# Kernel tuning notes

Hardware: AMD Instinct MI355X
Metric: run time of the kernel (lower is better)

Reference implementation:

```python
import jax, jax.numpy as jnp
import numpy as np

C = 1.0            # curvature
MIN_NORM = 1e-15   # hgcn min_norm
PROJ_EPS = 4e-3    # hgcn PoincareBall float32 boundary eps
N, D, E = 100000, 128, 1600000


def _artanh(x):
    # hgcn Artanh clamps input away from +-1 for stability
    return jnp.arctanh(jnp.clip(x, -1.0 + 1e-5, 1.0 - 1e-5))


def logmap0(p, c):
    sqrt_c = c ** 0.5
    p_norm = jnp.maximum(jnp.linalg.norm(p, axis=-1, keepdims=True), MIN_NORM)
    return p * _artanh(sqrt_c * p_norm) / (sqrt_c * p_norm)


def expmap0(u, c):
    sqrt_c = c ** 0.5
    u_norm = jnp.maximum(jnp.linalg.norm(u, axis=-1, keepdims=True), MIN_NORM)
    return jnp.tanh(sqrt_c * u_norm) * u / (sqrt_c * u_norm)


def proj(x, c):
    norm = jnp.maximum(jnp.linalg.norm(x, axis=-1, keepdims=True), MIN_NORM)
    maxnorm = (1.0 - PROJ_EPS) / (c ** 0.5)
    return jnp.where(norm > maxnorm, x / norm * maxnorm, x)


def setup_inputs() -> dict:
    key = jax.random.key(0)
    k1, k2, k3, k4 = jax.random.split(key, 4)
    # node features on the Poincare ball (small tangent vectors -> exp -> proj)
    x = proj(0.05 * jax.random.normal(k1, (N, D), dtype=jnp.float32), C)
    rows = jax.random.randint(k2, (E,), 0, N, dtype=jnp.int32)   # dst nodes
    cols = jax.random.randint(k3, (E,), 0, N, dtype=jnp.int32)   # src nodes
    # positive edge weights, roughly row-normalized (avg degree 16)
    vals = jax.random.uniform(k4, (E,), dtype=jnp.float32) / 16.0
    return {"x": x, "rows": rows, "cols": cols, "vals": vals}


def reference(x, rows, cols, vals):
    # x_tangent = logmap0(x)
    x_tangent = logmap0(x, C)                         # [N, D]
    # support_t = spmm(adj, x_tangent): gather src features, weight, scatter-add to dst
    msgs = vals[:, None] * x_tangent[cols]            # [E, D]
    support_t = jax.ops.segment_sum(msgs, rows, num_segments=N)  # [N, D]
    # output = proj(expmap0(support_t))
    return proj(expmap0(support_t, C), C)
```

## Files before the change

kernel.cpp:

```cpp
#include <hip/hip_runtime.h>
#include <hip/hip_fp16.h>
#include <math.h>

#define DIM 128
#define MAXNORM (1.0f - 4e-3f)
#define RPB 128
#define EPB 4096
#define CAP 64
#define CSTRIDE 32
#define SCAN_BLK 1024
#define GTHREADS 512

__device__ __forceinline__ float wave_reduce_sum(float v) {
    #pragma unroll
    for (int off = 32; off > 0; off >>= 1)
        v += __shfl_xor(v, off, 64);
    return v;
}

__device__ __forceinline__ float bf_lo(unsigned u) { return __uint_as_float(u << 16); }
__device__ __forceinline__ float bf_hi(unsigned u) { return __uint_as_float(u & 0xffff0000u); }

__device__ __forceinline__ unsigned pack_bf2(float a, float b) {
    unsigned ua = __float_as_uint(a), ub = __float_as_uint(b);
    ua += 0x7fffu + ((ua >> 16) & 1u);
    ub += 0x7fffu + ((ub >> 16) & 1u);
    return (ua >> 16) | (ub & 0xffff0000u);
}

__global__ void xt_kernel(const float* __restrict__ x,
                          unsigned* __restrict__ xt, int n) {
    int wave = (int)((blockIdx.x * blockDim.x + threadIdx.x) >> 6);
    int lane = threadIdx.x & 63;
    if (wave >= n) return;
    const float2* xr = (const float2*)(x + (size_t)wave * DIM);
    float2 v = xr[lane];
    float ss = wave_reduce_sum(v.x * v.x + v.y * v.y);
    float norm = sqrtf(ss);
    float t = fminf(norm, 1.0f - 1e-5f);
    float at = 0.5f * logf((1.0f + t) / (1.0f - t));
    float f = at / fmaxf(norm, 1e-15f);
    xt[(size_t)wave * 64 + lane] = pack_bf2(v.x * f, v.y * f);
}

__global__ void hist_part_kernel(const int* __restrict__ rows,
                                 int* __restrict__ hist, int E, int NB) {
    extern __shared__ int lh[];
    int tid = threadIdx.x;
    for (int i = tid; i < NB; i += 256) lh[i] = 0;
    __syncthreads();
    int base = blockIdx.x * EPB;
    for (int k = 0; k < EPB; k += 256) {
        int e = base + k + tid;
        if (e < E) atomicAdd(&lh[rows[e] >> 7], 1);
    }
    __syncthreads();
    int* h = hist + (size_t)blockIdx.x * NB;
    for (int i = tid; i < NB; i += 256) h[i] = lh[i];
}

__global__ void colscan_kernel(int* __restrict__ hist, int* __restrict__ bucketTotal,
                               int NEB, int NB) {
    int b = blockIdx.x * 64 + threadIdx.x;
    if (b >= NB) return;
    int carry = 0;
    int blk = 0;
    for (; blk + 8 <= NEB; blk += 8) {
        int v[8];
        #pragma unroll
        for (int k = 0; k < 8; k++) v[k] = hist[(size_t)(blk + k) * NB + b];
        #pragma unroll
        for (int k = 0; k < 8; k++) { hist[(size_t)(blk + k) * NB + b] = carry; carry += v[k]; }
    }
    for (; blk < NEB; blk++) {
        int v = hist[(size_t)blk * NB + b];
        hist[(size_t)blk * NB + b] = carry; carry += v;
    }
    bucketTotal[b] = carry;
}

__global__ void excl_scan_kernel(const int* __restrict__ src, int* __restrict__ dst, int nb) {
    __shared__ int s[SCAN_BLK];
    int tid = threadIdx.x;
    int v0 = (tid < nb) ? src[tid] : 0;
    s[tid] = v0; __syncthreads();
    for (int off = 1; off < SCAN_BLK; off <<= 1) {
        int v = (tid >= off) ? s[tid - off] : 0; __syncthreads();
        s[tid] += v; __syncthreads();
    }
    if (tid < nb) dst[tid] = s[tid] - v0;
}

__global__ void reorder_kernel(const int* __restrict__ rows, const int* __restrict__ cols,
                               const float* __restrict__ vals,
                               const int* __restrict__ hist,
                               const int* __restrict__ bucketBase,
                               uint2* __restrict__ records, int E, int NB) {
    extern __shared__ int sm[];
    int* s        = sm;
    int* locStart = sm + SCAN_BLK;
    int* locCur   = locStart + NB;
    int* gbase    = locCur + NB;
    uint2* stage  = (uint2*)(gbase + NB);
    int tid = threadIdx.x;
    int base = blockIdx.x * EPB;
    int nloc = E - base; if (nloc > EPB) nloc = EPB;

    for (int i = tid; i < NB; i += SCAN_BLK) locCur[i] = 0;
    __syncthreads();
    for (int k = 0; k < EPB; k += SCAN_BLK) {
        int e = base + k + tid;
        if (e < E) atomicAdd(&locCur[rows[e] >> 7], 1);
    }
    __syncthreads();
    int v0 = (tid < NB) ? locCur[tid] : 0;
    s[tid] = v0; __syncthreads();
    for (int off = 1; off < SCAN_BLK; off <<= 1) {
        int v = (tid >= off) ? s[tid - off] : 0; __syncthreads();
        s[tid] += v; __syncthreads();
    }
    int excl = s[tid] - v0;
    if (tid < NB) {
        locStart[tid] = excl;
        locCur[tid]   = excl;
        gbase[tid]    = bucketBase[tid] + hist[(size_t)blockIdx.x * NB + tid];
    }
    __syncthreads();
    for (int k = 0; k < EPB; k += SCAN_BLK) {
        int e = base + k + tid;
        if (e < E) {
            int r = rows[e];
            int b = r >> 7;
            unsigned hw = (unsigned)__half_as_ushort(__float2half(vals[e])) & 0x7fffu;
            unsigned pk = ((unsigned)cols[e] << 15) | hw;
            int p = atomicAdd(&locCur[b], 1);
            stage[p] = make_uint2(pk, (unsigned)r);
        }
    }
    __syncthreads();
    for (int i = tid; i < nloc; i += SCAN_BLK) {
        uint2 rec = stage[i];
        int b = (int)(rec.y >> 7);
        int rank = i - locStart[b];
        records[(size_t)gbase[b] + rank] = rec;
    }
}

__global__ void bucket_gather_kernel(const unsigned* __restrict__ xt,
                                     const uint2* __restrict__ records,
                                     const int* __restrict__ bucketBase,
                                     const int* __restrict__ bucketTotal,
                                     float* __restrict__ out, int n) {
    __shared__ unsigned ell[RPB * CAP];
    __shared__ int cnt[RPB];
    int b = blockIdx.x;
    int tid = threadIdx.x;
    int row0 = b * RPB;
    int rowsInB = n - row0; if (rowsInB > RPB) rowsInB = RPB;
    for (int i = tid; i < RPB; i += GTHREADS) cnt[i] = 0;
    __syncthreads();
    int e0 = bucketBase[b];
    int e1 = e0 + bucketTotal[b];
    for (int i = e0 + tid; i < e1; i += GTHREADS) {
        uint2 rec = records[i];
        int lr = (int)(rec.y & (RPB - 1));
        int p = atomicAdd(&cnt[lr], 1);
        if (p < CAP) ell[lr * CAP + p] = rec.x;
    }
    __syncthreads();
    int wv = tid >> 6, lane = tid & 63;
    for (int lr = wv; lr < rowsInB; lr += GTHREADS / 64) {
        int deg = cnt[lr]; if (deg > CAP) deg = CAP;
        float2 acc = make_float2(0.f, 0.f);
        const unsigned* erow = &ell[lr * CAP];
        for (int j = 0; j < deg; j += 8) {
            float w[8]; unsigned u[8]; int c[8];
            #pragma unroll
            for (int k = 0; k < 8; k++) {
                int idx = j + k;
                bool ok = idx < deg;
                unsigned p = erow[ok ? idx : 0];
                c[k] = (int)(p >> 15);
                w[k] = ok ? __half2float(__ushort_as_half((unsigned short)(p & 0x7fffu))) : 0.f;
            }
            #pragma unroll
            for (int k = 0; k < 8; k++) u[k] = xt[(size_t)c[k] * 64 + lane];
            #pragma unroll
            for (int k = 0; k < 8; k++) {
                acc.x = fmaf(w[k], bf_lo(u[k]), acc.x);
                acc.y = fmaf(w[k], bf_hi(u[k]), acc.y);
            }
        }
        float ss = wave_reduce_sum(acc.x * acc.x + acc.y * acc.y);
        float n0 = fmaxf(sqrtf(ss), 1e-15f);
        float th = tanhf(n0);
        float f = (th > MAXNORM) ? (MAXNORM / n0) : (th / n0);
        float2* o = (float2*)(out + (size_t)(row0 + lr) * DIM);
        o[lane] = make_float2(acc.x * f, acc.y * f);
    }
}

__global__ void scatter_ell_kernel(const int* __restrict__ rows,
                                   const int* __restrict__ cols,
                                   const float* __restrict__ vals,
                                   int* __restrict__ cur,
                                   unsigned* __restrict__ ell, int E) {
    int e = blockIdx.x * blockDim.x + threadIdx.x;
    if (e >= E) return;
    int r = rows[e];
    unsigned hb = (unsigned)__half_as_ushort(__float2half(vals[e])) & 0x7fffu;
    unsigned pk = ((unsigned)cols[e] << 15) | hb;
    int pos = atomicAdd(&cur[(size_t)r * CSTRIDE], 1);
    if (pos < CAP) ell[(size_t)r * CAP + pos] = pk;
}

__global__ void gather_ell_kernel(const unsigned* __restrict__ xt,
                                  const unsigned* __restrict__ ell,
                                  const int* __restrict__ cur,
                                  float* __restrict__ out, int n) {
    int wave = (int)((blockIdx.x * blockDim.x + threadIdx.x) >> 6);
    int lane = threadIdx.x & 63;
    if (wave >= n) return;
    int deg = cur[(size_t)wave * CSTRIDE];
    if (deg > CAP) deg = CAP;
    unsigned pl = 0;
    if (lane < deg) pl = ell[(size_t)wave * CAP + lane];
    float2 acc = make_float2(0.f, 0.f);
    for (int j = 0; j < deg; j += 8) {
        float w[8]; unsigned u[8]; int c[8];
        #pragma unroll
        for (int k = 0; k < 8; k++) {
            int idx = j + k;
            bool ok = idx < deg;
            unsigned p = __shfl(pl, ok ? idx : 0);
            c[k] = (int)(p >> 15);
            w[k] = ok ? __half2float(__ushort_as_half((unsigned short)(p & 0x7fffu))) : 0.f;
        }
        #pragma unroll
        for (int k = 0; k < 8; k++)
            u[k] = xt[(size_t)c[k] * 64 + lane];
        #pragma unroll
        for (int k = 0; k < 8; k++) {
            acc.x = fmaf(w[k], bf_lo(u[k]), acc.x);
            acc.y = fmaf(w[k], bf_hi(u[k]), acc.y);
        }
    }
    float ss = wave_reduce_sum(acc.x * acc.x + acc.y * acc.y);
    float n0 = fmaxf(sqrtf(ss), 1e-15f);
    float th = tanhf(n0);
    float f = (th > MAXNORM) ? (MAXNORM / n0) : (th / n0);
    float2* o = (float2*)(out + (size_t)wave * DIM);
    o[lane] = make_float2(acc.x * f, acc.y * f);
}

__global__ void tangent_kernel(const float* __restrict__ x,
                               float* __restrict__ xt, int n) {
    int wave = (int)((blockIdx.x * blockDim.x + threadIdx.x) >> 6);
    int lane = threadIdx.x & 63;
    if (wave >= n) return;
    const float2* xr = (const float2*)(x + (size_t)wave * DIM);
    float2 v = xr[lane];
    float ss = wave_reduce_sum(v.x * v.x + v.y * v.y);
    float norm = sqrtf(ss);
    float t = fminf(norm, 1.0f - 1e-5f);
    float at = 0.5f * logf((1.0f + t) / (1.0f - t));
    float factor = at / fmaxf(norm, 1e-15f);
    float2* o = (float2*)(xt + (size_t)wave * DIM);
    o[lane] = make_float2(v.x * factor, v.y * factor);
}

__global__ void scatter_kernel(const float* __restrict__ xt,
                               const int* __restrict__ rows,
                               const int* __restrict__ cols,
                               const float* __restrict__ vals,
                               float* __restrict__ out, int E) {
    long gid = (long)blockIdx.x * blockDim.x + threadIdx.x;
    int e = (int)(gid >> 5);
    int lane = (int)(gid & 31);
    if (e >= E) return;
    int r = rows[e];
    int c = cols[e];
    float w = vals[e];
    const float4* src = (const float4*)(xt + (size_t)c * DIM);
    float4 v = src[lane];
    float* dst = out + (size_t)r * DIM + lane * 4;
    unsafeAtomicAdd(dst + 0, v.x * w);
    unsafeAtomicAdd(dst + 1, v.y * w);
    unsafeAtomicAdd(dst + 2, v.z * w);
    unsafeAtomicAdd(dst + 3, v.w * w);
}

__global__ void finalize_kernel(float* __restrict__ out, int n) {
    int wave = (int)((blockIdx.x * blockDim.x + threadIdx.x) >> 6);
    int lane = threadIdx.x & 63;
    if (wave >= n) return;
    float2* p = (float2*)(out + (size_t)wave * DIM);
    float2 v = p[lane];
    float ss = wave_reduce_sum(v.x * v.x + v.y * v.y);
    float n0 = fmaxf(sqrtf(ss), 1e-15f);
    float th = tanhf(n0);
    float factor = (th > MAXNORM) ? (MAXNORM / n0) : (th / n0);
    p[lane] = make_float2(v.x * factor, v.y * factor);
}

extern "C" void kernel_launch(void* const* d_in, const int* in_sizes, int n_in,
                              void* d_out, int out_size, void* d_ws, size_t ws_size,
                              hipStream_t stream) {
    const float* x    = (const float*)d_in[0];
    const int*   rows = (const int*)d_in[1];
    const int*   cols = (const int*)d_in[2];
    const float* vals = (const float*)d_in[3];
    float* out = (float*)d_out;

    int n = in_sizes[0] / DIM;
    int E = in_sizes[1];
    int NB  = (n + RPB - 1) / RPB;
    int NEB = (E + EPB - 1) / EPB;

    auto align256 = [](size_t b) { return (b + 255) & ~(size_t)255; };

    size_t xt_b   = align256((size_t)n * 64 * 4);
    size_t rec_b  = align256((size_t)E * 8);
    size_t hist_b = align256((size_t)NEB * NB * 4);
    size_t bt_b   = align256((size_t)NB * 4);
    size_t bb_b   = align256((size_t)NB * 4);
    size_t radix_need = xt_b + rec_b + hist_b + bt_b + bb_b;
    size_t reorder_lds = (size_t)(SCAN_BLK + 3 * NB) * 4 + (size_t)EPB * 8;

    if (n <= (1 << 17) && NB <= SCAN_BLK && E > 0 &&
        reorder_lds <= 64 * 1024 && radix_need <= ws_size) {
        unsigned* xt_bf = (unsigned*)d_ws;
        uint2*    recs  = (uint2*)((char*)d_ws + xt_b);
        int*      hist  = (int*)((char*)d_ws + xt_b + rec_b);
        int*      btot  = (int*)((char*)d_ws + xt_b + rec_b + hist_b);
        int*      bbase = (int*)((char*)d_ws + xt_b + rec_b + hist_b + bt_b);

        xt_kernel<<<(n + 3) / 4, 256, 0, stream>>>(x, xt_bf, n);
        hist_part_kernel<<<NEB, 256, NB * 4, stream>>>(rows, hist, E, NB);
        colscan_kernel<<<(NB + 63) / 64, 64, 0, stream>>>(hist, btot, NEB, NB);
        excl_scan_kernel<<<1, SCAN_BLK, 0, stream>>>(btot, bbase, NB);
        reorder_kernel<<<NEB, SCAN_BLK, reorder_lds, stream>>>(rows, cols, vals,
                                                               hist, bbase, recs, E, NB);
        bucket_gather_kernel<<<NB, GTHREADS, 0, stream>>>(xt_bf, recs, bbase, btot, out, n);
        return;
    }

    size_t ell_b = align256((size_t)n * CAP * 4);
    size_t cur_b = align256((size_t)n * CSTRIDE * 4);
    if (n <= (1 << 17) && xt_b + ell_b + cur_b <= ws_size) {
        unsigned* xt_bf = (unsigned*)d_ws;
        unsigned* ell   = (unsigned*)((char*)d_ws + xt_b);
        int*      cur   = (int*)((char*)d_ws + xt_b + ell_b);
        xt_kernel<<<(n + 3) / 4, 256, 0, stream>>>(x, xt_bf, n);
        hipMemsetAsync(cur, 0, (size_t)n * CSTRIDE * 4, stream);
        scatter_ell_kernel<<<(E + 255) / 256, 256, 0, stream>>>(rows, cols, vals, cur, ell, E);
        gather_ell_kernel<<<(n + 3) / 4, 256, 0, stream>>>(xt_bf, ell, cur, out, n);
        return;
    }

    float* xtf = (float*)d_in[0];
    size_t xtb = (size_t)n * DIM * sizeof(float);
    if (ws_size >= xtb) xtf = (float*)d_ws;
    tangent_kernel<<<(n + 3) / 4, 256, 0, stream>>>(x, xtf, n);
    hipMemsetAsync(d_out, 0, (size_t)n * DIM * sizeof(float), stream);
    long threads = (long)E * 32;
    scatter_kernel<<<(int)((threads + 255) / 256), 256, 0, stream>>>(xtf, rows, cols, vals, out, E);
    finalize_kernel<<<(n + 3) / 4, 256, 0, stream>>>(out, n);
}
```

Measured before the change: 239.6 us.

## Use fp16 tangent features, atomic bucket offsets, and split gather blocks

Tangent features are now stored as fp16 pairs instead of bf16. The per-block histogram with its column scan is replaced by global atomic bucket totals and atomic cursor reservation in the reorder pass, which drops two kernels and the hist buffer. The gather kernel now runs two blocks per bucket, each handling 64 rows. It uses launch bounds, zero-pads ELL rows so they can be read with vectorized uint4 loads, and computes byte offsets directly. In exchange, each record list is read twice, edge order within a bucket is no longer deterministic, and fp16 has a narrower range than bf16.

```diff
diff --git a/kernel.cpp b/kernel.cpp
--- a/kernel.cpp
+++ b/kernel.cpp
@@ -5,6 +5,7 @@
 #define DIM 128
 #define MAXNORM (1.0f - 4e-3f)
 #define RPB 128
+#define GRPB 64
 #define EPB 4096
 #define CAP 64
 #define CSTRIDE 32
@@ -18,14 +19,10 @@
     return v;
 }
 
-__device__ __forceinline__ float bf_lo(unsigned u) { return __uint_as_float(u << 16); }
-__device__ __forceinline__ float bf_hi(unsigned u) { return __uint_as_float(u & 0xffff0000u); }
-
-__device__ __forceinline__ unsigned pack_bf2(float a, float b) {
-    unsigned ua = __float_as_uint(a), ub = __float_as_uint(b);
-    ua += 0x7fffu + ((ua >> 16) & 1u);
-    ub += 0x7fffu + ((ub >> 16) & 1u);
-    return (ua >> 16) | (ub & 0xffff0000u);
+__device__ __forceinline__ unsigned pack_h2(float a, float b) {
+    unsigned lo = (unsigned)__half_as_ushort(__float2half_rn(a));
+    unsigned hi = (unsigned)__half_as_ushort(__float2half_rn(b));
+    return lo | (hi << 16);
 }
 
 __global__ void xt_kernel(const float* __restrict__ x,
@@ -40,11 +37,11 @@
     float t = fminf(norm, 1.0f - 1e-5f);
     float at = 0.5f * logf((1.0f + t) / (1.0f - t));
     float f = at / fmaxf(norm, 1e-15f);
-    xt[(size_t)wave * 64 + lane] = pack_bf2(v.x * f, v.y * f);
-}
-
-__global__ void hist_part_kernel(const int* __restrict__ rows,
-                                 int* __restrict__ hist, int E, int NB) {
+    xt[(size_t)wave * 64 + lane] = pack_h2(v.x * f, v.y * f);
+}
+
+__global__ void hist_atomic_kernel(const int* __restrict__ rows,
+                                   int* __restrict__ btot, int E, int NB) {
     extern __shared__ int lh[];
     int tid = threadIdx.x;
     for (int i = tid; i < NB; i += 256) lh[i] = 0;
@@ -55,46 +52,27 @@
         if (e < E) atomicAdd(&lh[rows[e] >> 7], 1);
     }
     __syncthreads();
-    int* h = hist + (size_t)blockIdx.x * NB;
-    for (int i = tid; i < NB; i += 256) h[i] = lh[i];
-}
-
-__global__ void colscan_kernel(int* __restrict__ hist, int* __restrict__ bucketTotal,
-                               int NEB, int NB) {
-    int b = blockIdx.x * 64 + threadIdx.x;
-    if (b >= NB) return;
-    int carry = 0;
-    int blk = 0;
-    for (; blk + 8 <= NEB; blk += 8) {
-        int v[8];
-        #pragma unroll
-        for (int k = 0; k < 8; k++) v[k] = hist[(size_t)(blk + k) * NB + b];
-        #pragma unroll
-        for (int k = 0; k < 8; k++) { hist[(size_t)(blk + k) * NB + b] = carry; carry += v[k]; }
-    }
-    for (; blk < NEB; blk++) {
-        int v = hist[(size_t)blk * NB + b];
-        hist[(size_t)blk * NB + b] = carry; carry += v;
-    }
-    bucketTotal[b] = carry;
-}
-
-__global__ void excl_scan_kernel(const int* __restrict__ src, int* __restrict__ dst, int nb) {
+    for (int i = tid; i < NB; i += 256)
+        if (lh[i]) atomicAdd(&btot[i], lh[i]);
+}
+
+__global__ void scan_init_kernel(const int* __restrict__ btot,
+                                 int* __restrict__ bbase,
+                                 int* __restrict__ bcur, int nb) {
     __shared__ int s[SCAN_BLK];
     int tid = threadIdx.x;
-    int v0 = (tid < nb) ? src[tid] : 0;
+    int v0 = (tid < nb) ? btot[tid] : 0;
     s[tid] = v0; __syncthreads();
     for (int off = 1; off < SCAN_BLK; off <<= 1) {
         int v = (tid >= off) ? s[tid - off] : 0; __syncthreads();
         s[tid] += v; __syncthreads();
     }
-    if (tid < nb) dst[tid] = s[tid] - v0;
+    if (tid < nb) { int e = s[tid] - v0; bbase[tid] = e; bcur[tid] = e; }
 }
 
 __global__ void reorder_kernel(const int* __restrict__ rows, const int* __restrict__ cols,
                                const float* __restrict__ vals,
-                               const int* __restrict__ hist,
-                               const int* __restrict__ bucketBase,
+                               int* __restrict__ bucketCur,
                                uint2* __restrict__ records, int E, int NB) {
     extern __shared__ int sm[];
     int* s        = sm;
@@ -123,7 +101,7 @@
     if (tid < NB) {
         locStart[tid] = excl;
         locCur[tid]   = excl;
-        gbase[tid]    = bucketBase[tid] + hist[(size_t)blockIdx.x * NB + tid];
+        gbase[tid]    = atomicAdd(&bucketCur[tid], v0);
     }
     __syncthreads();
     for (int k = 0; k < EPB; k += SCAN_BLK) {
@@ -146,57 +124,70 @@
     }
 }
 
-__global__ void bucket_gather_kernel(const unsigned* __restrict__ xt,
-                                     const uint2* __restrict__ records,
-                                     const int* __restrict__ bucketBase,
-                                     const int* __restrict__ bucketTotal,
-                                     float* __restrict__ out, int n) {
-    __shared__ unsigned ell[RPB * CAP];
-    __shared__ int cnt[RPB];
-    int b = blockIdx.x;
+__global__ void __launch_bounds__(GTHREADS, 8)
+bucket_gather_kernel(const unsigned* __restrict__ xt,
+                     const uint2* __restrict__ records,
+                     const int* __restrict__ bucketBase,
+                     const int* __restrict__ bucketTotal,
+                     float* __restrict__ out, int n) {
+    __shared__ unsigned ell[GRPB * CAP];
+    __shared__ int cnt[GRPB];
+    int g = blockIdx.x;
+    int b = g >> 1, h = g & 1;
     int tid = threadIdx.x;
-    int row0 = b * RPB;
-    int rowsInB = n - row0; if (rowsInB > RPB) rowsInB = RPB;
-    for (int i = tid; i < RPB; i += GTHREADS) cnt[i] = 0;
+    int row0 = b * RPB + h * GRPB;
+    int rowsInB = n - row0; if (rowsInB > GRPB) rowsInB = GRPB;
+    for (int i = tid; i < GRPB; i += GTHREADS) cnt[i] = 0;
     __syncthreads();
     int e0 = bucketBase[b];
     int e1 = e0 + bucketTotal[b];
     for (int i = e0 + tid; i < e1; i += GTHREADS) {
         uint2 rec = records[i];
-        int lr = (int)(rec.y & (RPB - 1));
-        int p = atomicAdd(&cnt[lr], 1);
-        if (p < CAP) ell[lr * CAP + p] = rec.x;
+        if ((int)((rec.y >> 6) & 1u) == h) {
+            int lr = (int)(rec.y & (GRPB - 1));
+            int p = atomicAdd(&cnt[lr], 1);
+            if (p < CAP) ell[lr * CAP + p] = rec.x;
+        }
+    }
+    __syncthreads();
+    if (tid < GRPB) {
+        int d = cnt[tid]; if (d > CAP) d = CAP;
+        int dp = (d + 7) & ~7; if (dp > CAP) dp = CAP;
+        for (int ss = d; ss < dp; ++ss) ell[tid * CAP + ss] = 0;
     }
     __syncthreads();
     int wv = tid >> 6, lane = tid & 63;
+    unsigned lane4 = (unsigned)(lane << 2);
     for (int lr = wv; lr < rowsInB; lr += GTHREADS / 64) {
         int deg = cnt[lr]; if (deg > CAP) deg = CAP;
-        float2 acc = make_float2(0.f, 0.f);
+        float ax = 0.f, ay = 0.f;
         const unsigned* erow = &ell[lr * CAP];
         for (int j = 0; j < deg; j += 8) {
-            float w[8]; unsigned u[8]; int c[8];
+            uint4 qa = *(const uint4*)(erow + j);
+            uint4 qb = *(const uint4*)(erow + j + 4);
+            unsigned pk[8] = {qa.x, qa.y, qa.z, qa.w, qb.x, qb.y, qb.z, qb.w};
+            __half2 u[8];
+            float w[8];
             #pragma unroll
             for (int k = 0; k < 8; k++) {
-                int idx = j + k;
-                bool ok = idx < deg;
-                unsigned p = erow[ok ? idx : 0];
-                c[k] = (int)(p >> 15);
-                w[k] = ok ? __half2float(__ushort_as_half((unsigned short)(p & 0x7fffu))) : 0.f;
+                unsigned voff = ((pk[k] >> 15) << 8) + lane4;
+                u[k] = *(const __half2*)((const char*)xt + voff);
             }
             #pragma unroll
-            for (int k = 0; k < 8; k++) u[k] = xt[(size_t)c[k] * 64 + lane];
+            for (int k = 0; k < 8; k++)
+                w[k] = __half2float(__ushort_as_half((unsigned short)(pk[k] & 0x7fffu)));
             #pragma unroll
             for (int k = 0; k < 8; k++) {
-                acc.x = fmaf(w[k], bf_lo(u[k]), acc.x);
-                acc.y = fmaf(w[k], bf_hi(u[k]), acc.y);
+                ax = fmaf(w[k], __low2float(u[k]), ax);
+                ay = fmaf(w[k], __high2float(u[k]), ay);
             }
         }
-        float ss = wave_reduce_sum(acc.x * acc.x + acc.y * acc.y);
-        float n0 = fmaxf(sqrtf(ss), 1e-15f);
+        float ssum = wave_reduce_sum(ax * ax + ay * ay);
+        float n0 = fmaxf(sqrtf(ssum), 1e-15f);
         float th = tanhf(n0);
         float f = (th > MAXNORM) ? (MAXNORM / n0) : (th / n0);
         float2* o = (float2*)(out + (size_t)(row0 + lr) * DIM);
-        o[lane] = make_float2(acc.x * f, acc.y * f);
+        o[lane] = make_float2(ax * f, ay * f);
     }
 }
 
@@ -221,13 +212,14 @@
     int wave = (int)((blockIdx.x * blockDim.x + threadIdx.x) >> 6);
     int lane = threadIdx.x & 63;
     if (wave >= n) return;
+    const __half2* xt2 = (const __half2*)xt;
     int deg = cur[(size_t)wave * CSTRIDE];
     if (deg > CAP) deg = CAP;
     unsigned pl = 0;
     if (lane < deg) pl = ell[(size_t)wave * CAP + lane];
     float2 acc = make_float2(0.f, 0.f);
     for (int j = 0; j < deg; j += 8) {
-        float w[8]; unsigned u[8]; int c[8];
+        float w[8]; __half2 u[8]; int c[8];
         #pragma unroll
         for (int k = 0; k < 8; k++) {
             int idx = j + k;
@@ -238,11 +230,11 @@
         }
         #pragma unroll
         for (int k = 0; k < 8; k++)
-            u[k] = xt[(size_t)c[k] * 64 + lane];
+            u[k] = xt2[(size_t)c[k] * 64 + lane];
         #pragma unroll
         for (int k = 0; k < 8; k++) {
-            acc.x = fmaf(w[k], bf_lo(u[k]), acc.x);
-            acc.y = fmaf(w[k], bf_hi(u[k]), acc.y);
+            acc.x = fmaf(w[k], __low2float(u[k]), acc.x);
+            acc.y = fmaf(w[k], __high2float(u[k]), acc.y);
         }
     }
     float ss = wave_reduce_sum(acc.x * acc.x + acc.y * acc.y);
@@ -319,42 +311,40 @@
 
     auto align256 = [](size_t b) { return (b + 255) & ~(size_t)255; };
 
-    size_t xt_b   = align256((size_t)n * 64 * 4);
-    size_t rec_b  = align256((size_t)E * 8);
-    size_t hist_b = align256((size_t)NEB * NB * 4);
-    size_t bt_b   = align256((size_t)NB * 4);
-    size_t bb_b   = align256((size_t)NB * 4);
-    size_t radix_need = xt_b + rec_b + hist_b + bt_b + bb_b;
+    size_t xt_b  = align256((size_t)n * 64 * 4);
+    size_t rec_b = align256((size_t)E * 8);
+    size_t nb_b  = align256((size_t)NB * 4);
+    size_t radix_need = xt_b + rec_b + 3 * nb_b;
     size_t reorder_lds = (size_t)(SCAN_BLK + 3 * NB) * 4 + (size_t)EPB * 8;
 
     if (n <= (1 << 17) && NB <= SCAN_BLK && E > 0 &&
         reorder_lds <= 64 * 1024 && radix_need <= ws_size) {
-        unsigned* xt_bf = (unsigned*)d_ws;
+        unsigned* xt_h  = (unsigned*)d_ws;
         uint2*    recs  = (uint2*)((char*)d_ws + xt_b);
-        int*      hist  = (int*)((char*)d_ws + xt_b + rec_b);
-        int*      btot  = (int*)((char*)d_ws + xt_b + rec_b + hist_b);
-        int*      bbase = (int*)((char*)d_ws + xt_b + rec_b + hist_b + bt_b);
-
-        xt_kernel<<<(n + 3) / 4, 256, 0, stream>>>(x, xt_bf, n);
-        hist_part_kernel<<<NEB, 256, NB * 4, stream>>>(rows, hist, E, NB);
-        colscan_kernel<<<(NB + 63) / 64, 64, 0, stream>>>(hist, btot, NEB, NB);
-        excl_scan_kernel<<<1, SCAN_BLK, 0, stream>>>(btot, bbase, NB);
+        int*      btot  = (int*)((char*)d_ws + xt_b + rec_b);
+        int*      bbase = (int*)((char*)d_ws + xt_b + rec_b + nb_b);
+        int*      bcur  = (int*)((char*)d_ws + xt_b + rec_b + 2 * nb_b);
+
+        hipMemsetAsync(btot, 0, (size_t)NB * 4, stream);
+        xt_kernel<<<(n + 3) / 4, 256, 0, stream>>>(x, xt_h, n);
+        hist_atomic_kernel<<<NEB, 256, NB * 4, stream>>>(rows, btot, E, NB);
+        scan_init_kernel<<<1, SCAN_BLK, 0, stream>>>(btot, bbase, bcur, NB);
         reorder_kernel<<<NEB, SCAN_BLK, reorder_lds, stream>>>(rows, cols, vals,
-                                                               hist, bbase, recs, E, NB);
-        bucket_gather_kernel<<<NB, GTHREADS, 0, stream>>>(xt_bf, recs, bbase, btot, out, n);
+                                                               bcur, recs, E, NB);
+        bucket_gather_kernel<<<NB * 2, GTHREADS, 0, stream>>>(xt_h, recs, bbase, btot, out, n);
         return;
     }
 
     size_t ell_b = align256((size_t)n * CAP * 4);
     size_t cur_b = align256((size_t)n * CSTRIDE * 4);
     if (n <= (1 << 17) && xt_b + ell_b + cur_b <= ws_size) {
-        unsigned* xt_bf = (unsigned*)d_ws;
-        unsigned* ell   = (unsigned*)((char*)d_ws + xt_b);
-        int*      cur   = (int*)((char*)d_ws + xt_b + ell_b);
-        xt_kernel<<<(n + 3) / 4, 256, 0, stream>>>(x, xt_bf, n);
+        unsigned* xt_h = (unsigned*)d_ws;
+        unsigned* ell  = (unsigned*)((char*)d_ws + xt_b);
+        int*      cur  = (int*)((char*)d_ws + xt_b + ell_b);
+        xt_kernel<<<(n + 3) / 4, 256, 0, stream>>>(x, xt_h, n);
         hipMemsetAsync(cur, 0, (size_t)n * CSTRIDE * 4, stream);
         scatter_ell_kernel<<<(E + 255) / 256, 256, 0, stream>>>(rows, cols, vals, cur, ell, E);
-        gather_ell_kernel<<<(n + 3) / 4, 256, 0, stream>>>(xt_bf, ell, cur, out, n);
+        gather_ell_kernel<<<(n + 3) / 4, 256, 0, stream>>>(xt_h, ell, cur, out, n);
         return;
     }
 
```

Measured after the change: 219.5 us. -8.4%, faster.
